# Optimization experiments

Measured on AMD Instinct MI355X. Metric: run time of the kernel, lower is better.

## Reference

```python
import jax, jax.numpy as jnp
import numpy as np

Q_HEADS, KV_HEADS, DIMS = 16, 4, 1024
HEAD_DIM = DIMS // Q_HEADS          # 64
GROUPS = Q_HEADS // KV_HEADS        # 4
ROPE_BASE = 10000.0


def rope(x):
    # x: (..., s, d) -- standard interleaved rotary embedding, base 10000
    s, d = x.shape[-2], x.shape[-1]
    inv_freq = 1.0 / (ROPE_BASE ** (jnp.arange(0, d, 2, dtype=jnp.float32) / d))
    ang = jnp.arange(s, dtype=jnp.float32)[:, None] * inv_freq[None, :]  # (s, d/2)
    cos, sin = jnp.cos(ang), jnp.sin(ang)
    x1, x2 = x[..., 0::2], x[..., 1::2]
    out = jnp.stack([x1 * cos - x2 * sin, x1 * sin + x2 * cos], axis=-1)
    return out.reshape(x.shape).astype(x.dtype)


def setup_inputs() -> dict:
    key = jax.random.key(0)
    k1, k2, k3, k4, k5, k6 = jax.random.split(key, 6)
    B, S, E = 4, 2048, 1024
    q = jax.random.normal(k1, (B, S, E), dtype=jnp.float32)
    kv = jax.random.normal(k2, (B, S, E), dtype=jnp.float32)
    sc = 1.0 / np.sqrt(E)
    Wq = jax.random.normal(k3, (E, Q_HEADS, HEAD_DIM), dtype=jnp.float32) * sc
    Wk = jax.random.normal(k4, (E, KV_HEADS, HEAD_DIM), dtype=jnp.float32) * sc
    Wv = jax.random.normal(k5, (E, KV_HEADS, HEAD_DIM), dtype=jnp.float32) * sc
    Wo = jax.random.normal(k6, (HEAD_DIM, E), dtype=jnp.float32) / np.sqrt(HEAD_DIM)
    return {"q": q, "kv": kv, "Wq": Wq, "Wk": Wk, "Wv": Wv, "Wo": Wo}


def reference(q, kv, Wq, Wk, Wv, Wo):
    B, S, E = q.shape
    qh = jnp.einsum('bse,ehd->bshd', q, Wq)    # (B,S,Q_HEADS,hd)
    kh = jnp.einsum('bse,ehd->bshd', kv, Wk)   # (B,S,KV_HEADS,hd)
    vh = jnp.einsum('bse,ehd->bshd', kv, Wv)
    # rearrange '... s (h g) d -> ... g h s d' with g=GROUPS (h = KV_HEADS outer)
    qh = qh.reshape(B, S, KV_HEADS, GROUPS, HEAD_DIM).transpose(0, 3, 2, 1, 4)  # (B,g,h,S,d)
    kh = kh.transpose(0, 2, 1, 3)  # (B,h,S,d)
    vh = vh.transpose(0, 2, 1, 3)  # (B,h,S,d)
    qh = rope(qh)
    kh = rope(kh)
    # NOTE: sums over group axis g (faithful to original einsum)
    scores = jnp.einsum('bghsd,bhad->bhsa', qh, kh)
    attn = jax.nn.softmax(scores / (HEAD_DIM ** 0.5), axis=-1)
    out = jnp.einsum('bhsa,bhad->bhsd', attn, vh)  # (B,h,S,d)
    out = out.mean(axis=1)                          # mean over kv heads -> (B,S,d)
    return out @ Wo                                 # (B,S,E)
```

## Files before the change

kernel.cpp:

```cpp
#include <hip/hip_runtime.h>
#include <math.h>

#define SS 2048
#define EE 1024

using bf16x8 = __attribute__((ext_vector_type(8))) short;
using f32x4  = __attribute__((ext_vector_type(4))) float;

__device__ inline short f2bf(float x) {
    unsigned u = __builtin_bit_cast(unsigned, x);
    return (short)((u + 0x7fffu + ((u >> 16) & 1u)) >> 16);
}
__device__ inline short f2bf_r(float x) {
    return (short)((__builtin_bit_cast(unsigned, x) + 0x8000u) >> 16);
}
__device__ inline unsigned pk_bf16(float a, float b) {
    unsigned ua = __builtin_bit_cast(unsigned, a) + 0x8000u;
    unsigned ub = __builtin_bit_cast(unsigned, b) + 0x8000u;
    return __builtin_amdgcn_perm(ub, ua, 0x07060302u);
}
__device__ inline void gl16(const short* g, short* l) {
    __builtin_amdgcn_global_load_lds(
        (const __attribute__((address_space(1))) void*)g,
        (__attribute__((address_space(3))) void*)l, 16, 0, 0);
}

__global__ __launch_bounds__(256) void prep_weights(const float* __restrict__ q,
                                                    const float* __restrict__ kv,
                                                    const float* __restrict__ Wq,
                                                    const float* __restrict__ Wk,
                                                    const float* __restrict__ Wv,
                                                    const float* __restrict__ Wo,
                                                    short* __restrict__ Ab,
                                                    short* __restrict__ Wall,
                                                    short* __restrict__ Wo4,
                                                    float2* __restrict__ RT) {
    if (blockIdx.x < 8192) {
        int gt = blockIdx.x * 256 + threadIdx.x;
        size_t e0 = (size_t)gt * 8;
        const float* src = (e0 < 8388608) ? (q + e0) : (kv + (e0 - 8388608));
        float4 v0 = *(const float4*)src;
        float4 v1 = *(const float4*)(src + 4);
        int4 u;
        u.x = pk_bf16(v0.x, v0.y);
        u.y = pk_bf16(v0.z, v0.w);
        u.z = pk_bf16(v1.x, v1.y);
        u.w = pk_bf16(v1.z, v1.w);
        *(int4*)&Ab[e0] = u;
        return;
    }
    int idx = (blockIdx.x - 8192) * 256 + threadIdx.x;
    int c = idx >> 10, e = idx & 1023;
    int h = c >> 6, d = c & 63;
    const float* p = Wq + (size_t)e * 1024 + h * 256 + d;
    Wall[(size_t)c * 1024 + e] = f2bf(0.18033688011112042f * (p[0] + p[64] + p[128] + p[192]));
    Wall[(size_t)(256 + c) * 1024 + e] = f2bf(Wk[(size_t)e * 256 + c]);
    Wall[(size_t)(512 + c) * 1024 + e] = f2bf(Wv[(size_t)e * 256 + c]);
    Wo4[(size_t)e * 256 + c] = f2bf(0.25f * Wo[(size_t)d * 1024 + e]);
    if (idx < 65536) {
        int s = idx >> 5, ii = idx & 31;
        float freq = __expf(-(float)ii * (9.210340371976184f / 32.0f));
        float sn, cs;
        sincosf((float)s * freq, &sn, &cs);
        RT[idx] = (float2){cs, sn};
    }
}

__global__ __launch_bounds__(256) void proj_kernel(const short* __restrict__ Ab,
                                                   const short* __restrict__ Wall,
                                                   const float2* __restrict__ RT,
                                                   short* __restrict__ Qb,
                                                   short* __restrict__ Kb,
                                                   short* __restrict__ Vt) {
    __shared__ alignas(16) short SMEM[128 * 64 + 64 * 64];
    short (*As)[64] = (short (*)[64])SMEM;
    short (*Bs)[64] = (short (*)[64])(SMEM + 128 * 64);
    int tid = threadIdx.x;
    int wave = tid >> 6, lane = tid & 63, quad = lane >> 4, c16 = lane & 15;
    int wm = wave >> 1, wn = wave & 1;
    int m0 = blockIdx.x * 128, n0 = blockIdx.y * 64;
    const short* A = Ab + ((n0 < 256) ? 0 : (size_t)8388608);

    int lr = lane >> 3, lc = lane & 7;
    f32x4 acc[4][2];
    #pragma unroll
    for (int i = 0; i < 4; i++)
        #pragma unroll
        for (int j = 0; j < 2; j++) acc[i][j] = (f32x4){0.f, 0.f, 0.f, 0.f};

    for (int k0 = 0; k0 < 1024; k0 += 64) {
        __syncthreads();
        #pragma unroll
        for (int i = 0; i < 4; i++) {
            int seg = wave * 4 + i;
            int r = seg * 8 + lr;
            gl16(&A[(size_t)(m0 + r) * 1024 + k0 + lc * 8], &As[seg * 8][0]);
        }
        #pragma unroll
        for (int i = 0; i < 2; i++) {
            int seg = wave * 2 + i;
            int r = seg * 8 + lr;
            gl16(&Wall[(size_t)(n0 + r) * 1024 + k0 + lc * 8], &Bs[seg * 8][0]);
        }
        __syncthreads();
        #pragma unroll
        for (int ks = 0; ks < 64; ks += 32) {
            bf16x8 af[4], bfr[2];
            #pragma unroll
            for (int mt = 0; mt < 4; mt++)
                af[mt] = *(const bf16x8*)&As[wm * 64 + mt * 16 + c16][ks + quad * 8];
            #pragma unroll
            for (int nt = 0; nt < 2; nt++)
                bfr[nt] = *(const bf16x8*)&Bs[wn * 32 + nt * 16 + c16][ks + quad * 8];
            #pragma unroll
            for (int mt = 0; mt < 4; mt++)
                #pragma unroll
                for (int nt = 0; nt < 2; nt++)
                    acc[mt][nt] = __builtin_amdgcn_mfma_f32_16x16x32_bf16(
                        af[mt], bfr[nt], acc[mt][nt], 0, 0, 0);
        }
    }
    __syncthreads();
    if (n0 < 512) {
        #pragma unroll
        for (int mt = 0; mt < 4; mt++) {
            #pragma unroll
            for (int nt = 0; nt < 2; nt++) {
                int cl = wn * 32 + nt * 16 + c16;
                int ii = cl >> 1;
                float sgn = (lane & 1) ? 1.0f : -1.0f;
                f32x4 v = acc[mt][nt];
                #pragma unroll
                for (int r = 0; r < 4; r++) {
                    int rl = wm * 64 + mt * 16 + quad * 4 + r;
                    float2 cs = RT[((m0 + rl) & (SS - 1)) * 32 + ii];
                    float other = __shfl_xor(v[r], 1);
                    As[rl][cl] = f2bf_r(v[r] * cs.x + sgn * cs.y * other);
                }
            }
        }
        __syncthreads();
        short* dstb = (n0 < 256) ? Qb : Kb;
        int nc0 = n0 & 255;
        #pragma unroll
        for (int i = 0; i < 4; i++) {
            int id = i * 256 + tid, r = id >> 3, ch = id & 7;
            *(int4*)&dstb[(size_t)(m0 + r) * 256 + nc0 + ch * 8] =
                *(const int4*)&As[r][ch * 8];
        }
    } else {
        short (*Lt)[136] = (short(*)[136])SMEM;
        #pragma unroll
        for (int mt = 0; mt < 4; mt++) {
            #pragma unroll
            for (int nt = 0; nt < 2; nt++) {
                int cl = wn * 32 + nt * 16 + c16;
                int sl = wm * 64 + mt * 16 + quad * 4;
                f32x4 v = acc[mt][nt];
                uint2 u;
                u.x = pk_bf16(v[0], v[1]);
                u.y = pk_bf16(v[2], v[3]);
                *(uint2*)&Lt[cl][sl] = u;
            }
        }
        __syncthreads();
        int b = m0 >> 11, s0 = m0 & (SS - 1), c0 = n0 - 512;
        #pragma unroll
        for (int i = 0; i < 4; i++) {
            int id = i * 256 + tid, c = id >> 4, ch = id & 15;
            *(int4*)&Vt[((size_t)(b * 256 + c0 + c)) * SS + s0 + ch * 8] =
                *(const int4*)&Lt[c][ch * 8];
        }
    }
}

__global__ __launch_bounds__(512, 4) void attn_kernel(const short* __restrict__ Qb,
                                                      const short* __restrict__ Kb,
                                                      const short* __restrict__ Vt,
                                                      short* __restrict__ Ob) {
    __shared__ alignas(16) short Qs[64][72];
    __shared__ alignas(16) short Ps2[64][72];
    __shared__ alignas(16) short Ks[2][64][72];
    __shared__ alignas(16) short Vs[2][64][72];
    int tid = threadIdx.x;
    int wave = tid >> 6, lane = tid & 63, quad = lane >> 4, c16 = lane & 15;
    int rq = wave & 3, kh = wave >> 2;
    int qt = blockIdx.x, bh = blockIdx.y;
    int q0 = qt * 64;
    size_t qkbase = (size_t)(bh >> 2) * SS * 256 + (bh & 3) * 64;
    size_t vtbase = (size_t)(bh * 64) * SS;

    {
        int r = tid >> 3, ch = tid & 7;
        *(int4*)&Qs[r][ch * 8] = *(const int4*)&Qb[qkbase + (size_t)(q0 + r) * 256 + ch * 8];
    }
    __syncthreads();
    bf16x8 aq0 = *(const bf16x8*)&Qs[rq * 16 + c16][quad * 8];
    bf16x8 aq1 = *(const bf16x8*)&Qs[rq * 16 + c16][32 + quad * 8];
    short (*Ps)[72] = (kh == 0) ? (short (*)[72])Qs[rq * 16] : (short (*)[72])Ps2[rq * 16];

    float lsum[4] = {0.f, 0.f, 0.f, 0.f};
    f32x4 o[4];
    #pragma unroll
    for (int dt = 0; dt < 4; dt++) o[dt] = (f32x4){0.f, 0.f, 0.f, 0.f};

    int sr = tid >> 3, sch = tid & 7;
    int4 kr0 = *(const int4*)&Kb[qkbase + (size_t)sr * 256 + sch * 8];
    int4 kr1 = *(const int4*)&Kb[qkbase + (size_t)(1024 + sr) * 256 + sch * 8];
    int4 vr0 = *(const int4*)&Vt[vtbase + (size_t)sr * SS + sch * 8];
    int4 vr1 = *(const int4*)&Vt[vtbase + (size_t)sr * SS + 1024 + sch * 8];

    for (int kt = 0; kt < 16; kt++) {
        __syncthreads();
        *(int4*)&Ks[0][sr][sch * 8] = kr0;
        *(int4*)&Ks[1][sr][sch * 8] = kr1;
        *(int4*)&Vs[0][sr][sch * 8] = vr0;
        *(int4*)&Vs[1][sr][sch * 8] = vr1;
        if (kt < 15) {
            int a1 = (kt + 1) * 64;
            kr0 = *(const int4*)&Kb[qkbase + (size_t)(a1 + sr) * 256 + sch * 8];
            kr1 = *(const int4*)&Kb[qkbase + (size_t)(1024 + a1 + sr) * 256 + sch * 8];
            vr0 = *(const int4*)&Vt[vtbase + (size_t)sr * SS + a1 + sch * 8];
            vr1 = *(const int4*)&Vt[vtbase + (size_t)sr * SS + 1024 + a1 + sch * 8];
        }
        __syncthreads();
        f32x4 sv[4];
        #pragma unroll
        for (int nt = 0; nt < 4; nt++) sv[nt] = (f32x4){0.f, 0.f, 0.f, 0.f};
        #pragma unroll
        for (int nt = 0; nt < 4; nt++) {
            bf16x8 bk0 = *(const bf16x8*)&Ks[kh][nt * 16 + c16][quad * 8];
            bf16x8 bk1 = *(const bf16x8*)&Ks[kh][nt * 16 + c16][32 + quad * 8];
            sv[nt] = __builtin_amdgcn_mfma_f32_16x16x32_bf16(aq0, bk0, sv[nt], 0, 0, 0);
            sv[nt] = __builtin_amdgcn_mfma_f32_16x16x32_bf16(aq1, bk1, sv[nt], 0, 0, 0);
        }
        #pragma unroll
        for (int nt = 0; nt < 4; nt++)
            #pragma unroll
            for (int r = 0; r < 4; r++) sv[nt][r] = __builtin_exp2f(sv[nt][r]);
        #pragma unroll
        for (int r = 0; r < 4; r++)
            lsum[r] += (sv[0][r] + sv[1][r]) + (sv[2][r] + sv[3][r]);
        #pragma unroll
        for (int nt = 0; nt < 4; nt++)
            #pragma unroll
            for (int r = 0; r < 4; r++)
                Ps[quad * 4 + r][nt * 16 + c16] = f2bf_r(sv[nt][r]);
        #pragma unroll
        for (int ks = 0; ks < 64; ks += 32) {
            bf16x8 ap = *(const bf16x8*)&Ps[c16][ks + quad * 8];
            #pragma unroll
            for (int dt = 0; dt < 4; dt++) {
                bf16x8 bv = *(const bf16x8*)&Vs[kh][dt * 16 + c16][ks + quad * 8];
                o[dt] = __builtin_amdgcn_mfma_f32_16x16x32_bf16(ap, bv, o[dt], 0, 0, 0);
            }
        }
    }
    #pragma unroll
    for (int off = 1; off < 16; off <<= 1)
        #pragma unroll
        for (int r = 0; r < 4; r++) lsum[r] += __shfl_xor(lsum[r], off);

    __syncthreads();
    float (*Ox)[68] = (float (*)[68])&Ks[0][0][0];
    float* Lx = (float*)&Vs[0][0][0];
    short (*Ot)[72] = (short (*)[72])&Vs[1][0][0];
    int base = rq * 16 + quad * 4;
    if (wave >= 4) {
        #pragma unroll
        for (int dt = 0; dt < 4; dt++)
            #pragma unroll
            for (int r = 0; r < 4; r++)
                Ox[base + r][dt * 16 + c16] = o[dt][r];
        if (c16 == 0)
            #pragma unroll
            for (int r = 0; r < 4; r++) Lx[base + r] = lsum[r];
    }
    __syncthreads();
    if (wave < 4) {
        #pragma unroll
        for (int r = 0; r < 4; r++) {
            float rl = __builtin_amdgcn_rcpf(lsum[r] + Lx[base + r]);
            #pragma unroll
            for (int dt = 0; dt < 4; dt++)
                Ot[base + r][dt * 16 + c16] =
                    f2bf_r((o[dt][r] + Ox[base + r][dt * 16 + c16]) * rl);
        }
    }
    __syncthreads();
    {
        int r = tid >> 3, ch = tid & 7;
        int b = bh >> 2, h = bh & 3;
        *(int4*)&Ob[((size_t)(b * SS + q0 + r)) * 256 + h * 64 + ch * 8] =
            *(const int4*)&Ot[r][ch * 8];
    }
}

__global__ __launch_bounds__(256) void outproj_kernel(const short* __restrict__ Ob,
                                                      const short* __restrict__ Wo4,
                                                      float* __restrict__ out) {
    __shared__ alignas(16) short As[128][72];
    __shared__ alignas(16) short Bs[64][72];
    int tid = threadIdx.x;
    int wave = tid >> 6, lane = tid & 63, quad = lane >> 4, c16 = lane & 15;
    int m0 = blockIdx.x * 128, n0 = blockIdx.y * 64;

    f32x4 acc[2][4];
    #pragma unroll
    for (int i = 0; i < 2; i++)
        #pragma unroll
        for (int j = 0; j < 4; j++) acc[i][j] = (f32x4){0.f, 0.f, 0.f, 0.f};

    for (int k0 = 0; k0 < 256; k0 += 64) {
        #pragma unroll
        for (int i = 0; i < 4; i++) {
            int id = i * 256 + tid, r = id >> 3, ch = id & 7;
            *(int4*)&As[r][ch * 8] =
                *(const int4*)&Ob[(size_t)(m0 + r) * 256 + k0 + ch * 8];
        }
        #pragma unroll
        for (int i = 0; i < 2; i++) {
            int id = i * 256 + tid, r = id >> 3, ch = id & 7;
            *(int4*)&Bs[r][ch * 8] =
                *(const int4*)&Wo4[(size_t)(n0 + r) * 256 + k0 + ch * 8];
        }
        __syncthreads();
        #pragma unroll
        for (int ks = 0; ks < 64; ks += 32) {
            bf16x8 af[2], bfr[4];
            #pragma unroll
            for (int mt = 0; mt < 2; mt++)
                af[mt] = *(const bf16x8*)&As[wave * 32 + mt * 16 + c16][ks + quad * 8];
            #pragma unroll
            for (int nt = 0; nt < 4; nt++)
                bfr[nt] = *(const bf16x8*)&Bs[nt * 16 + c16][ks + quad * 8];
            #pragma unroll
            for (int mt = 0; mt < 2; mt++)
                #pragma unroll
                for (int nt = 0; nt < 4; nt++)
                    acc[mt][nt] = __builtin_amdgcn_mfma_f32_16x16x32_bf16(
                        af[mt], bfr[nt], acc[mt][nt], 0, 0, 0);
        }
        __syncthreads();
    }
    #pragma unroll
    for (int mt = 0; mt < 2; mt++)
        #pragma unroll
        for (int nt = 0; nt < 4; nt++) {
            int col = n0 + nt * 16 + c16;
            int rowb = m0 + wave * 32 + mt * 16 + quad * 4;
            #pragma unroll
            for (int r = 0; r < 4; r++)
                out[(size_t)(rowb + r) * 1024 + col] = acc[mt][nt][r];
        }
}

extern "C" void kernel_launch(void* const* d_in, const int* in_sizes, int n_in,
                              void* d_out, int out_size, void* d_ws, size_t ws_size,
                              hipStream_t stream) {
    const float* q  = (const float*)d_in[0];
    const float* kv = (const float*)d_in[1];
    const float* Wq = (const float*)d_in[2];
    const float* Wk = (const float*)d_in[3];
    const float* Wv = (const float*)d_in[4];
    const float* Wo = (const float*)d_in[5];
    float* out = (float*)d_out;

    short* Qb    = (short*)d_ws;
    short* Kb    = Qb + 2097152;
    short* Vt    = Kb + 2097152;
    short* Wall  = Vt + 2097152;
    short* Wo4   = Wall + 786432;
    float2* RT   = (float2*)(Wo4 + 262144);
    short* Ob    = (short*)(RT + 65536);
    short* Ab    = Ob + 2097152;

    prep_weights<<<9216, 256, 0, stream>>>(q, kv, Wq, Wk, Wv, Wo, Ab, Wall, Wo4, RT);

    proj_kernel<<<dim3(64, 12), 256, 0, stream>>>(Ab, Wall, RT, Qb, Kb, Vt);

    attn_kernel<<<dim3(32, 16), 512, 0, stream>>>(Qb, Kb, Vt, Ob);

    outproj_kernel<<<dim3(64, 16), 256, 0, stream>>>(Ob, Wo4, out);
}
```

Before: 194.5 us.

## Load Q/K/V MFMA fragments directly from global memory, drop LDS staging

The attention kernel no longer stages K and V tiles into shared memory behind block-wide barriers. Each wave now loads its MFMA operand fragments for Q, K and V straight from global memory, and the only LDS left is per-wave P buffers plus a small reduction scratch. This removes two __syncthreads per key tile and the LDS write/read traffic, and it cuts shared-memory use, which may allow higher occupancy. In exchange, the four query waves that share a K/V tile each fetch it separately from global memory or cache, with no explicit prefetch to hide that latency.

```diff
diff --git a/kernel.cpp b/kernel.cpp
--- a/kernel.cpp
+++ b/kernel.cpp
@@ -178,10 +178,9 @@
                                                       const short* __restrict__ Kb,
                                                       const short* __restrict__ Vt,
                                                       short* __restrict__ Ob) {
-    __shared__ alignas(16) short Qs[64][72];
-    __shared__ alignas(16) short Ps2[64][72];
-    __shared__ alignas(16) short Ks[2][64][72];
-    __shared__ alignas(16) short Vs[2][64][72];
+    __shared__ alignas(16) short Psb[8][16][72];
+    __shared__ alignas(16) short Otb[64][72];
+    __shared__ float Lxb[64];
     int tid = threadIdx.x;
     int wave = tid >> 6, lane = tid & 63, quad = lane >> 4, c16 = lane & 15;
     int rq = wave & 3, kh = wave >> 2;
@@ -190,47 +189,30 @@
     size_t qkbase = (size_t)(bh >> 2) * SS * 256 + (bh & 3) * 64;
     size_t vtbase = (size_t)(bh * 64) * SS;
 
-    {
-        int r = tid >> 3, ch = tid & 7;
-        *(int4*)&Qs[r][ch * 8] = *(const int4*)&Qb[qkbase + (size_t)(q0 + r) * 256 + ch * 8];
-    }
-    __syncthreads();
-    bf16x8 aq0 = *(const bf16x8*)&Qs[rq * 16 + c16][quad * 8];
-    bf16x8 aq1 = *(const bf16x8*)&Qs[rq * 16 + c16][32 + quad * 8];
-    short (*Ps)[72] = (kh == 0) ? (short (*)[72])Qs[rq * 16] : (short (*)[72])Ps2[rq * 16];
+    const short* qrow = Qb + qkbase + (size_t)(q0 + rq * 16 + c16) * 256 + quad * 8;
+    bf16x8 aq0 = *(const bf16x8*)qrow;
+    bf16x8 aq1 = *(const bf16x8*)(qrow + 32);
+
+    short (*Ps)[72] = Psb[wave];
+
+    const short* kp = Kb + qkbase + (size_t)(kh * 1024 + c16) * 256 + quad * 8;
+    const short* vp = Vt + vtbase + (size_t)c16 * SS + kh * 1024 + quad * 8;
 
     float lsum[4] = {0.f, 0.f, 0.f, 0.f};
     f32x4 o[4];
     #pragma unroll
     for (int dt = 0; dt < 4; dt++) o[dt] = (f32x4){0.f, 0.f, 0.f, 0.f};
 
-    int sr = tid >> 3, sch = tid & 7;
-    int4 kr0 = *(const int4*)&Kb[qkbase + (size_t)sr * 256 + sch * 8];
-    int4 kr1 = *(const int4*)&Kb[qkbase + (size_t)(1024 + sr) * 256 + sch * 8];
-    int4 vr0 = *(const int4*)&Vt[vtbase + (size_t)sr * SS + sch * 8];
-    int4 vr1 = *(const int4*)&Vt[vtbase + (size_t)sr * SS + 1024 + sch * 8];
-
     for (int kt = 0; kt < 16; kt++) {
-        __syncthreads();
-        *(int4*)&Ks[0][sr][sch * 8] = kr0;
-        *(int4*)&Ks[1][sr][sch * 8] = kr1;
-        *(int4*)&Vs[0][sr][sch * 8] = vr0;
-        *(int4*)&Vs[1][sr][sch * 8] = vr1;
-        if (kt < 15) {
-            int a1 = (kt + 1) * 64;
-            kr0 = *(const int4*)&Kb[qkbase + (size_t)(a1 + sr) * 256 + sch * 8];
-            kr1 = *(const int4*)&Kb[qkbase + (size_t)(1024 + a1 + sr) * 256 + sch * 8];
-            vr0 = *(const int4*)&Vt[vtbase + (size_t)sr * SS + a1 + sch * 8];
-            vr1 = *(const int4*)&Vt[vtbase + (size_t)sr * SS + 1024 + a1 + sch * 8];
-        }
-        __syncthreads();
+        int a0 = kt * 64;
         f32x4 sv[4];
         #pragma unroll
         for (int nt = 0; nt < 4; nt++) sv[nt] = (f32x4){0.f, 0.f, 0.f, 0.f};
         #pragma unroll
         for (int nt = 0; nt < 4; nt++) {
-            bf16x8 bk0 = *(const bf16x8*)&Ks[kh][nt * 16 + c16][quad * 8];
-            bf16x8 bk1 = *(const bf16x8*)&Ks[kh][nt * 16 + c16][32 + quad * 8];
+            const short* kfr = kp + (size_t)(a0 + nt * 16) * 256;
+            bf16x8 bk0 = *(const bf16x8*)kfr;
+            bf16x8 bk1 = *(const bf16x8*)(kfr + 32);
             sv[nt] = __builtin_amdgcn_mfma_f32_16x16x32_bf16(aq0, bk0, sv[nt], 0, 0, 0);
             sv[nt] = __builtin_amdgcn_mfma_f32_16x16x32_bf16(aq1, bk1, sv[nt], 0, 0, 0);
         }
@@ -251,7 +233,7 @@
             bf16x8 ap = *(const bf16x8*)&Ps[c16][ks + quad * 8];
             #pragma unroll
             for (int dt = 0; dt < 4; dt++) {
-                bf16x8 bv = *(const bf16x8*)&Vs[kh][dt * 16 + c16][ks + quad * 8];
+                bf16x8 bv = *(const bf16x8*)(vp + (size_t)dt * 16 * SS + a0 + ks);
                 o[dt] = __builtin_amdgcn_mfma_f32_16x16x32_bf16(ap, bv, o[dt], 0, 0, 0);
             }
         }
@@ -262,9 +244,9 @@
         for (int r = 0; r < 4; r++) lsum[r] += __shfl_xor(lsum[r], off);
 
     __syncthreads();
-    float (*Ox)[68] = (float (*)[68])&Ks[0][0][0];
-    float* Lx = (float*)&Vs[0][0][0];
-    short (*Ot)[72] = (short (*)[72])&Vs[1][0][0];
+    float (*Ox)[68] = (float (*)[68])&Psb[0][0][0];
+    float* Lx = Lxb;
+    short (*Ot)[72] = Otb;
     int base = rq * 16 + quad * 4;
     if (wave >= 4) {
         #pragma unroll
```

Result: slower. 274.1 us (+41.0%).
